# Kernel optimization log

Measured on AMD Instinct MI355X. Metric: run time of the kernel, lower is better.

## Reference

```python
import jax, jax.numpy as jnp
import numpy as np

N_HEADS = 16
D_MODEL = 1024
HEAD_DIM = D_MODEL // N_HEADS
B, S = 2, 2048


def setup_inputs() -> dict:
    key = jax.random.key(0)
    ks = jax.random.split(key, 10)
    scale = 1.0 / np.sqrt(D_MODEL)
    inp = {
        "query_tokens": jax.random.normal(ks[0], (B, S, D_MODEL), dtype=jnp.float32),
        "key_or_value_tokens": jax.random.normal(ks[1], (B, S, D_MODEL), dtype=jnp.float32),
        "mask": jnp.ones((B, S, S), dtype=jnp.int32),
        "Wq": jax.random.normal(ks[2], (D_MODEL, D_MODEL), dtype=jnp.float32) * scale,
        "bq": jnp.zeros((D_MODEL,), dtype=jnp.float32),
        "Wk": jax.random.normal(ks[3], (D_MODEL, D_MODEL), dtype=jnp.float32) * scale,
        "bk": jnp.zeros((D_MODEL,), dtype=jnp.float32),
        "Wv": jax.random.normal(ks[4], (D_MODEL, D_MODEL), dtype=jnp.float32) * scale,
        "bv": jnp.zeros((D_MODEL,), dtype=jnp.float32),
        "Wo": jax.random.normal(ks[5], (D_MODEL, D_MODEL), dtype=jnp.float32) * scale,
        "bo": jnp.zeros((D_MODEL,), dtype=jnp.float32),
    }
    return inp


def reference(query_tokens, key_or_value_tokens, mask, Wq, bq, Wk, bk, Wv, bv, Wo, bo):
    b, s, d = query_tokens.shape
    h, dh = N_HEADS, HEAD_DIM

    def proj(x, W, bias):
        # torch Linear: x @ W.T + b ; then split heads -> (b, h, s, dh)
        y = jnp.einsum("bsd,ed->bse", x, W) + bias
        return y.reshape(b, -1, h, dh).transpose(0, 2, 1, 3)

    q = proj(query_tokens, Wq, bq)
    k = proj(key_or_value_tokens, Wk, bk)
    v = proj(key_or_value_tokens, Wv, bv)

    scores = jnp.einsum("bhqd,bhkd->bhqk", q, k) / jnp.sqrt(jnp.float32(dh))
    # mask: (b, Sq, Sk) -> (b, 1, Sq, Sk); zeros get large negative fill
    scores = jnp.where(mask[:, None, :, :] == 0, jnp.float32(-1e9), scores)
    attn = jax.nn.softmax(scores, axis=-1)
    out = jnp.einsum("bhqk,bhkd->bhqd", attn, v)
    out = out.transpose(0, 2, 1, 3).reshape(b, s, d)
    return jnp.einsum("bsd,ed->bse", out, Wo) + bo
```

## Files before the change

### kernel.cpp

```cpp
#include <hip/hip_runtime.h>
#include <hip/hip_bf16.h>

typedef __bf16 bf16_8  __attribute__((ext_vector_type(8)));
typedef __bf16 bf16_4  __attribute__((ext_vector_type(4)));
typedef float  f32_4   __attribute__((ext_vector_type(4)));

#define NH 16
#define DHD 64
#define BB 2
#define SS 2048
#define DD 1024

__device__ __forceinline__ void gload16(const __bf16* g, __bf16* l) {
    __builtin_amdgcn_global_load_lds(
        (const __attribute__((address_space(1))) void*)g,
        (__attribute__((address_space(3))) void*)l, 16, 0, 0);
}

__global__ __launch_bounds__(256) void conv_all(
    const float* __restrict__ s0, const float* __restrict__ s1,
    const float* __restrict__ s2, const float* __restrict__ s3,
    const float* __restrict__ s4, const float* __restrict__ s5,
    __bf16* __restrict__ d0, __bf16* __restrict__ d1, __bf16* __restrict__ d2,
    __bf16* __restrict__ d3, __bf16* __restrict__ d4, __bf16* __restrict__ d5) {
    const int y = blockIdx.y;
    if (y >= 2 && blockIdx.x >= 1024) return;
    const float* s = (y == 0) ? s0 : (y == 1) ? s1 : (y == 2) ? s2
                   : (y == 3) ? s3 : (y == 4) ? s4 : s5;
    __bf16* d      = (y == 0) ? d0 : (y == 1) ? d1 : (y == 2) ? d2
                   : (y == 3) ? d3 : (y == 4) ? d4 : d5;
    const int i = (blockIdx.x * 256 + threadIdx.x) * 4;
    f32_4 v = *(const f32_4*)&s[i];
    bf16_4 o; o[0] = (__bf16)v[0]; o[1] = (__bf16)v[1];
    o[2] = (__bf16)v[2]; o[3] = (__bf16)v[3];
    *(bf16_4*)&d[i] = o;
}

__global__ __launch_bounds__(256) void mask_flags_k(const int* __restrict__ mask,
                                                    int* __restrict__ flags) {
    const int id = blockIdx.x;
    const int b = id >> 10, qt = (id >> 5) & 31, kt = id & 31;
    const int t = threadIdx.x;
    const int row = t >> 2, seg = t & 3;
    const int* p = mask + ((size_t)b * SS + qt * 64 + row) * SS + kt * 64 + seg * 16;
    int any0 = 0;
#pragma unroll
    for (int i = 0; i < 4; ++i) {
        int4 v = *(const int4*)&p[i * 4];
        any0 |= (v.x == 0) | (v.y == 0) | (v.z == 0) | (v.w == 0);
    }
    unsigned long long bal = __ballot(any0);
    __shared__ int sf[4];
    if ((t & 63) == 0) sf[t >> 6] = (bal != 0ULL);
    __syncthreads();
    if (t == 0) flags[id] = sf[0] | sf[1] | sf[2] | sf[3];
}

template <int LAYOUT>
__device__ __forceinline__ void gemm_body(const __bf16* __restrict__ A,
                                          const __bf16* __restrict__ W,
                                          const float* __restrict__ bias,
                                          __bf16* __restrict__ out,
                                          __bf16* ldsA, __bf16* ldsB) {
    const int tid  = threadIdx.x;
    const int lane = tid & 63;
    const int w    = tid >> 6;
    const int quad = lane >> 4;
    const int l15  = lane & 15;
    const int wm   = (w >> 1) * 64;
    const int wn   = (w & 1) * 64;
    const int m0   = blockIdx.x * 128;
    const int n0   = blockIdx.y * 128;

    f32_4 acc[4][4] = {};

    for (int kt = 0; kt < 1024; kt += 32) {
#pragma unroll
        for (int cc = 0; cc < 2; ++cc) {
            const int c   = tid + cc * 256;
            const int row = c >> 2;
            const int cp  = c & 3;
            gload16(&A[(size_t)(m0 + row) * 1024 + kt + cp * 8], &ldsA[c * 8]);
            gload16(&W[(size_t)(n0 + row) * 1024 + kt + cp * 8], &ldsB[c * 8]);
        }
        __syncthreads();

        bf16_8 af[4], bfr[4];
#pragma unroll
        for (int i = 0; i < 4; ++i)
            af[i] = *(const bf16_8*)&ldsA[(wm + i * 16 + l15) * 32 + quad * 8];
#pragma unroll
        for (int j = 0; j < 4; ++j)
            bfr[j] = *(const bf16_8*)&ldsB[(wn + j * 16 + l15) * 32 + quad * 8];
#pragma unroll
        for (int i = 0; i < 4; ++i)
#pragma unroll
            for (int j = 0; j < 4; ++j)
                acc[i][j] = __builtin_amdgcn_mfma_f32_16x16x32_bf16(
                    af[i], bfr[j], acc[i][j], 0, 0, 0);
        __syncthreads();
    }

#pragma unroll
    for (int i = 0; i < 4; ++i) {
#pragma unroll
        for (int j = 0; j < 4; ++j) {
            const int col = n0 + wn + j * 16 + l15;
            const float bv = bias[col];
            if (LAYOUT == 2) {
                const int row0 = m0 + wm + i * 16 + quad * 4;
                bf16_4 pk;
#pragma unroll
                for (int r = 0; r < 4; ++r) pk[r] = (__bf16)(acc[i][j][r] + bv);
                const int bb = row0 >> 11, s0 = row0 & 2047;
                const int h = col >> 6, dh = col & 63;
                *(bf16_4*)&out[(((size_t)bb * NH + h) * DHD + dh) * SS + s0] = pk;
            } else {
#pragma unroll
                for (int r = 0; r < 4; ++r) {
                    const int row = m0 + wm + i * 16 + quad * 4 + r;
                    out[(((size_t)(row >> 11) * NH + (col >> 6)) * SS +
                         (row & 2047)) * DHD + (col & 63)] =
                        (__bf16)(acc[i][j][r] + bv);
                }
            }
        }
    }
}

__global__ __launch_bounds__(256) void gemm_qkv(
    const __bf16* __restrict__ Xq, const __bf16* __restrict__ Xkv,
    const __bf16* __restrict__ Wq, const float* __restrict__ bq,
    const __bf16* __restrict__ Wk, const float* __restrict__ bk,
    const __bf16* __restrict__ Wv, const float* __restrict__ bv,
    __bf16* __restrict__ Qo, __bf16* __restrict__ Ko, __bf16* __restrict__ VTo) {
    __shared__ __align__(16) __bf16 ldsA[128 * 32];
    __shared__ __align__(16) __bf16 ldsB[128 * 32];
    const int z = blockIdx.z;
    const __bf16* A    = (z == 0) ? Xq : Xkv;
    const __bf16* W    = (z == 0) ? Wq : (z == 1 ? Wk : Wv);
    const float* bias  = (z == 0) ? bq : (z == 1 ? bk : bv);
    if (z == 2)
        gemm_body<2>(A, W, bias, VTo, ldsA, ldsB);
    else
        gemm_body<0>(A, W, bias, (z == 0) ? Qo : Ko, ldsA, ldsB);
}

__global__ __launch_bounds__(256) void gemm_final(
    const __bf16* __restrict__ A, const __bf16* __restrict__ W,
    const float* __restrict__ bias, float* __restrict__ out) {
    __shared__ __align__(16) __bf16 ldsA[64 * 32];
    __shared__ __align__(16) __bf16 ldsB[64 * 32];
    const int tid  = threadIdx.x;
    const int lane = tid & 63;
    const int w    = tid >> 6;
    const int quad = lane >> 4;
    const int l15  = lane & 15;
    const int wm   = (w >> 1) * 32;
    const int wn   = (w & 1) * 32;
    const int m0   = blockIdx.x * 64;
    const int n0   = blockIdx.y * 64;

    const int isB = w >> 1;
    const __bf16* src = isB ? W : A;
    const int     bN  = isB ? n0 : m0;
    __bf16*       dst = isB ? ldsB : ldsA;
    const int     w2  = w & 1;

    f32_4 acc[2][2] = {};

    for (int kt = 0; kt < 1024; kt += 32) {
#pragma unroll
        for (int cc = 0; cc < 2; ++cc) {
            const int c   = w2 * 128 + cc * 64 + lane;
            const int row = c >> 2;
            const int cp  = c & 3;
            gload16(&src[(size_t)(bN + row) * 1024 + kt + cp * 8], &dst[c * 8]);
        }
        __syncthreads();

        bf16_8 af[2], bfr[2];
#pragma unroll
        for (int i = 0; i < 2; ++i)
            af[i] = *(const bf16_8*)&ldsA[(wm + i * 16 + l15) * 32 + quad * 8];
#pragma unroll
        for (int j = 0; j < 2; ++j)
            bfr[j] = *(const bf16_8*)&ldsB[(wn + j * 16 + l15) * 32 + quad * 8];
#pragma unroll
        for (int i = 0; i < 2; ++i)
#pragma unroll
            for (int j = 0; j < 2; ++j)
                acc[i][j] = __builtin_amdgcn_mfma_f32_16x16x32_bf16(
                    af[i], bfr[j], acc[i][j], 0, 0, 0);
        __syncthreads();
    }

#pragma unroll
    for (int i = 0; i < 2; ++i)
#pragma unroll
        for (int j = 0; j < 2; ++j) {
            const int col = n0 + wn + j * 16 + l15;
            const float bv = bias[col];
#pragma unroll
            for (int r = 0; r < 4; ++r) {
                const int row = m0 + wm + i * 16 + quad * 4 + r;
                out[(size_t)row * 1024 + col] = acc[i][j][r] + bv;
            }
        }
}

__global__ __launch_bounds__(256, 2) void flash_attn(
    const __bf16* __restrict__ Q, const __bf16* __restrict__ K,
    const __bf16* __restrict__ VT, const int* __restrict__ mask,
    const int* __restrict__ flags, __bf16* __restrict__ O) {
    __shared__ __align__(16) __bf16 ldsK[64 * 72];
    __shared__ __align__(16) __bf16 ldsVT[64 * 72];
    __shared__ __align__(16) __bf16 ldsP[128 * 72];

    const int tid  = threadIdx.x;
    const int lane = tid & 63;
    const int w    = tid >> 6;
    const int quad = lane >> 4;
    const int l15  = lane & 15;
    const int q0   = blockIdx.x * 128;
    const int bh   = blockIdx.y;
    const int b    = bh >> 4;

    const __bf16* Qb  = Q + (size_t)bh * SS * DHD;
    const __bf16* Kb  = K + (size_t)bh * SS * DHD;
    const __bf16* VTb = VT + (size_t)bh * DHD * SS;
    const int*    mb  = mask + (size_t)b * SS * SS;
    const int*    flb = flags + (size_t)b * 1024 + blockIdx.x * 64;

    bf16_8 qa[2][2];
#pragma unroll
    for (int mt = 0; mt < 2; ++mt)
#pragma unroll
        for (int ks = 0; ks < 2; ++ks) {
            bf16_8 t = *(const bf16_8*)&Qb[(size_t)(q0 + w * 32 + mt * 16 + l15) * DHD +
                                           ks * 32 + quad * 8];
#pragma unroll
            for (int e = 0; e < 8; ++e)
                qa[mt][ks][e] = (__bf16)((float)t[e] * 0.18033688011112042f);
        }

    f32_4 of[2][4] = {};
    float li[2][4] = {};

    const int r0 = tid >> 3;
    const int r1 = r0 + 32;
    const int cp = tid & 7;
    uint4 kr0 = *(const uint4*)&Kb[(size_t)r0 * DHD + cp * 8];
    uint4 kr1 = *(const uint4*)&Kb[(size_t)r1 * DHD + cp * 8];
    uint4 vr0 = *(const uint4*)&VTb[(size_t)r0 * SS + cp * 8];
    uint4 vr1 = *(const uint4*)&VTb[(size_t)r1 * SS + cp * 8];

    for (int k0 = 0; k0 < SS; k0 += 64) {
        *(uint4*)&ldsK[r0 * 72 + cp * 8]  = kr0;
        *(uint4*)&ldsK[r1 * 72 + cp * 8]  = kr1;
        *(uint4*)&ldsVT[r0 * 72 + cp * 8] = vr0;
        *(uint4*)&ldsVT[r1 * 72 + cp * 8] = vr1;
        if (k0 + 64 < SS) {
            const int kn = k0 + 64;
            kr0 = *(const uint4*)&Kb[(size_t)(kn + r0) * DHD + cp * 8];
            kr1 = *(const uint4*)&Kb[(size_t)(kn + r1) * DHD + cp * 8];
            vr0 = *(const uint4*)&VTb[(size_t)r0 * SS + kn + cp * 8];
            vr1 = *(const uint4*)&VTb[(size_t)r1 * SS + kn + cp * 8];
        }
        __syncthreads();

        const bool msk = ((flb[k0 >> 6] | flb[32 + (k0 >> 6)]) != 0);

        f32_4 sa[2][4] = {};
#pragma unroll
        for (int ks = 0; ks < 2; ++ks) {
            bf16_8 kb[4];
#pragma unroll
            for (int j = 0; j < 4; ++j)
                kb[j] = *(const bf16_8*)&ldsK[(j * 16 + l15) * 72 + ks * 32 + quad * 8];
#pragma unroll
            for (int mt = 0; mt < 2; ++mt)
#pragma unroll
                for (int j = 0; j < 4; ++j)
                    sa[mt][j] = __builtin_amdgcn_mfma_f32_16x16x32_bf16(
                        qa[mt][ks], kb[j], sa[mt][j], 0, 0, 0);
        }

        if (msk) {
#pragma unroll
            for (int mt = 0; mt < 2; ++mt)
#pragma unroll
                for (int j = 0; j < 4; ++j)
#pragma unroll
                    for (int r = 0; r < 4; ++r) {
                        const int qg = q0 + w * 32 + mt * 16 + quad * 4 + r;
                        const int kg = k0 + j * 16 + l15;
                        if (mb[(size_t)qg * SS + kg] == 0) sa[mt][j][r] = -1e9f;
                    }
        }

#pragma unroll
        for (int mt = 0; mt < 2; ++mt)
#pragma unroll
            for (int j = 0; j < 4; ++j)
#pragma unroll
                for (int r = 0; r < 4; ++r) {
                    const float p = exp2f(sa[mt][j][r]);
                    li[mt][r] += p;
                    ldsP[(w * 32 + mt * 16 + quad * 4 + r) * 72 + j * 16 + l15] =
                        (__bf16)p;
                }
        __syncthreads();

#pragma unroll
        for (int ks2 = 0; ks2 < 2; ++ks2) {
            bf16_8 pa[2], vb[4];
#pragma unroll
            for (int mt = 0; mt < 2; ++mt)
                pa[mt] = *(const bf16_8*)&ldsP[(w * 32 + mt * 16 + l15) * 72 +
                                               ks2 * 32 + quad * 8];
#pragma unroll
            for (int jo = 0; jo < 4; ++jo)
                vb[jo] = *(const bf16_8*)&ldsVT[(jo * 16 + l15) * 72 +
                                                ks2 * 32 + quad * 8];
#pragma unroll
            for (int mt = 0; mt < 2; ++mt)
#pragma unroll
                for (int jo = 0; jo < 4; ++jo)
                    of[mt][jo] = __builtin_amdgcn_mfma_f32_16x16x32_bf16(
                        pa[mt], vb[jo], of[mt][jo], 0, 0, 0);
        }
        __syncthreads();
    }

    const int hcol = (bh & 15) * 64;
#pragma unroll
    for (int mt = 0; mt < 2; ++mt)
#pragma unroll
        for (int r = 0; r < 4; ++r) {
            float ls = li[mt][r];
            ls += __shfl_xor(ls, 1);
            ls += __shfl_xor(ls, 2);
            ls += __shfl_xor(ls, 4);
            ls += __shfl_xor(ls, 8);
            const float inv = 1.0f / fmaxf(ls, 1e-37f);
            const int qg = q0 + w * 32 + mt * 16 + quad * 4 + r;
#pragma unroll
            for (int jo = 0; jo < 4; ++jo)
                O[((size_t)b * SS + qg) * DD + hcol + jo * 16 + l15] =
                    (__bf16)(of[mt][jo][r] * inv);
        }
}


extern "C" void kernel_launch(void* const* d_in, const int* in_sizes, int n_in,
                              void* d_out, int out_size, void* d_ws, size_t ws_size,
                              hipStream_t stream) {
    const float* xq   = (const float*)d_in[0];
    const float* xkv  = (const float*)d_in[1];
    const int*   mask = (const int*)d_in[2];
    const float* Wq   = (const float*)d_in[3];
    const float* bq   = (const float*)d_in[4];
    const float* Wk   = (const float*)d_in[5];
    const float* bk   = (const float*)d_in[6];
    const float* Wv   = (const float*)d_in[7];
    const float* bv   = (const float*)d_in[8];
    const float* Wo   = (const float*)d_in[9];
    const float* bo   = (const float*)d_in[10];

    __bf16* ws = (__bf16*)d_ws;
    const size_t big = (size_t)BB * SS * DD;
    const size_t wsz = (size_t)DD * DD;
    __bf16* Qw   = ws;
    __bf16* Kw   = Qw + big;
    __bf16* VTw  = Kw + big;
    __bf16* Aw   = VTw + big;
    __bf16* Xqb  = Aw + big;
    __bf16* Xkvb = Xqb + big;
    __bf16* Wqb  = Xkvb + big;
    __bf16* Wkb  = Wqb + wsz;
    __bf16* Wvb  = Wkb + wsz;
    __bf16* Wob  = Wvb + wsz;
    int* flags   = (int*)(Wob + wsz);

    conv_all<<<dim3(4096, 6), dim3(256), 0, stream>>>(xq, xkv, Wq, Wk, Wv, Wo,
                                                      Xqb, Xkvb, Wqb, Wkb, Wvb, Wob);
    mask_flags_k<<<dim3(2048), dim3(256), 0, stream>>>(mask, flags);
    gemm_qkv<<<dim3(32, 8, 3), dim3(256), 0, stream>>>(Xqb, Xkvb, Wqb, bq, Wkb, bk,
                                                       Wvb, bv, Qw, Kw, VTw);
    flash_attn<<<dim3(SS / 128, BB * NH), dim3(256), 0, stream>>>(Qw, Kw, VTw, mask,
                                                                  flags, Aw);
    gemm_final<<<dim3(64, 16), dim3(256), 0, stream>>>(Aw, Wob, bo, (float*)d_out);
}
```

Before: 268.1 us.

## Fuse mask-flag scan into conversion kernel, enlarge output GEMM tile, pad P stride

```diff
diff --git a/kernel.cpp b/kernel.cpp
--- a/kernel.cpp
+++ b/kernel.cpp
@@ -17,13 +17,34 @@
         (__attribute__((address_space(3))) void*)l, 16, 0, 0);
 }
 
-__global__ __launch_bounds__(256) void conv_all(
+__global__ __launch_bounds__(256) void conv_flags(
     const float* __restrict__ s0, const float* __restrict__ s1,
     const float* __restrict__ s2, const float* __restrict__ s3,
     const float* __restrict__ s4, const float* __restrict__ s5,
     __bf16* __restrict__ d0, __bf16* __restrict__ d1, __bf16* __restrict__ d2,
-    __bf16* __restrict__ d3, __bf16* __restrict__ d4, __bf16* __restrict__ d5) {
+    __bf16* __restrict__ d3, __bf16* __restrict__ d4, __bf16* __restrict__ d5,
+    const int* __restrict__ mask, int* __restrict__ flags) {
     const int y = blockIdx.y;
+    if (y == 6) {
+        if (blockIdx.x >= 2048) return;
+        const int id = blockIdx.x;
+        const int b = id >> 10, qt = (id >> 5) & 31, kt = id & 31;
+        const int t = threadIdx.x;
+        const int row = t >> 2, seg = t & 3;
+        const int* p = mask + ((size_t)b * SS + qt * 64 + row) * SS + kt * 64 + seg * 16;
+        int any0 = 0;
+#pragma unroll
+        for (int i = 0; i < 4; ++i) {
+            int4 v = *(const int4*)&p[i * 4];
+            any0 |= (v.x == 0) | (v.y == 0) | (v.z == 0) | (v.w == 0);
+        }
+        unsigned long long bal = __ballot(any0);
+        __shared__ int sf[4];
+        if ((t & 63) == 0) sf[t >> 6] = (bal != 0ULL);
+        __syncthreads();
+        if (t == 0) flags[id] = sf[0] | sf[1] | sf[2] | sf[3];
+        return;
+    }
     if (y >= 2 && blockIdx.x >= 1024) return;
     const float* s = (y == 0) ? s0 : (y == 1) ? s1 : (y == 2) ? s2
                    : (y == 3) ? s3 : (y == 4) ? s4 : s5;
@@ -34,26 +55,6 @@
     bf16_4 o; o[0] = (__bf16)v[0]; o[1] = (__bf16)v[1];
     o[2] = (__bf16)v[2]; o[3] = (__bf16)v[3];
     *(bf16_4*)&d[i] = o;
-}
-
-__global__ __launch_bounds__(256) void mask_flags_k(const int* __restrict__ mask,
-                                                    int* __restrict__ flags) {
-    const int id = blockIdx.x;
-    const int b = id >> 10, qt = (id >> 5) & 31, kt = id & 31;
-    const int t = threadIdx.x;
-    const int row = t >> 2, seg = t & 3;
-    const int* p = mask + ((size_t)b * SS + qt * 64 + row) * SS + kt * 64 + seg * 16;
-    int any0 = 0;
-#pragma unroll
-    for (int i = 0; i < 4; ++i) {
-        int4 v = *(const int4*)&p[i * 4];
-        any0 |= (v.x == 0) | (v.y == 0) | (v.z == 0) | (v.w == 0);
-    }
-    unsigned long long bal = __ballot(any0);
-    __shared__ int sf[4];
-    if ((t & 63) == 0) sf[t >> 6] = (bal != 0ULL);
-    __syncthreads();
-    if (t == 0) flags[id] = sf[0] | sf[1] | sf[2] | sf[3];
 }
 
 template <int LAYOUT>
@@ -149,45 +150,41 @@
 __global__ __launch_bounds__(256) void gemm_final(
     const __bf16* __restrict__ A, const __bf16* __restrict__ W,
     const float* __restrict__ bias, float* __restrict__ out) {
-    __shared__ __align__(16) __bf16 ldsA[64 * 32];
+    __shared__ __align__(16) __bf16 ldsA[128 * 32];
     __shared__ __align__(16) __bf16 ldsB[64 * 32];
     const int tid  = threadIdx.x;
     const int lane = tid & 63;
     const int w    = tid >> 6;
     const int quad = lane >> 4;
     const int l15  = lane & 15;
-    const int wm   = (w >> 1) * 32;
+    const int wm   = (w >> 1) * 64;
     const int wn   = (w & 1) * 32;
-    const int m0   = blockIdx.x * 64;
+    const int m0   = blockIdx.x * 128;
     const int n0   = blockIdx.y * 64;
 
-    const int isB = w >> 1;
-    const __bf16* src = isB ? W : A;
-    const int     bN  = isB ? n0 : m0;
-    __bf16*       dst = isB ? ldsB : ldsA;
-    const int     w2  = w & 1;
-
-    f32_4 acc[2][2] = {};
+    f32_4 acc[4][2] = {};
 
     for (int kt = 0; kt < 1024; kt += 32) {
 #pragma unroll
         for (int cc = 0; cc < 2; ++cc) {
-            const int c   = w2 * 128 + cc * 64 + lane;
+            const int c   = tid + cc * 256;
             const int row = c >> 2;
             const int cp  = c & 3;
-            gload16(&src[(size_t)(bN + row) * 1024 + kt + cp * 8], &dst[c * 8]);
-        }
-        __syncthreads();
-
-        bf16_8 af[2], bfr[2];
-#pragma unroll
-        for (int i = 0; i < 2; ++i)
+            gload16(&A[(size_t)(m0 + row) * 1024 + kt + cp * 8], &ldsA[c * 8]);
+        }
+        gload16(&W[(size_t)(n0 + (tid >> 2)) * 1024 + kt + (tid & 3) * 8],
+                &ldsB[tid * 8]);
+        __syncthreads();
+
+        bf16_8 af[4], bfr[2];
+#pragma unroll
+        for (int i = 0; i < 4; ++i)
             af[i] = *(const bf16_8*)&ldsA[(wm + i * 16 + l15) * 32 + quad * 8];
 #pragma unroll
         for (int j = 0; j < 2; ++j)
             bfr[j] = *(const bf16_8*)&ldsB[(wn + j * 16 + l15) * 32 + quad * 8];
 #pragma unroll
-        for (int i = 0; i < 2; ++i)
+        for (int i = 0; i < 4; ++i)
 #pragma unroll
             for (int j = 0; j < 2; ++j)
                 acc[i][j] = __builtin_amdgcn_mfma_f32_16x16x32_bf16(
@@ -196,7 +193,7 @@
     }
 
 #pragma unroll
-    for (int i = 0; i < 2; ++i)
+    for (int i = 0; i < 4; ++i)
 #pragma unroll
         for (int j = 0; j < 2; ++j) {
             const int col = n0 + wn + j * 16 + l15;
@@ -209,13 +206,14 @@
         }
 }
 
+#define PST 76
 __global__ __launch_bounds__(256, 2) void flash_attn(
     const __bf16* __restrict__ Q, const __bf16* __restrict__ K,
     const __bf16* __restrict__ VT, const int* __restrict__ mask,
     const int* __restrict__ flags, __bf16* __restrict__ O) {
     __shared__ __align__(16) __bf16 ldsK[64 * 72];
     __shared__ __align__(16) __bf16 ldsVT[64 * 72];
-    __shared__ __align__(16) __bf16 ldsP[128 * 72];
+    __shared__ __align__(16) __bf16 ldsP[128 * PST];
 
     const int tid  = threadIdx.x;
     const int lane = tid & 63;
@@ -307,7 +305,7 @@
                 for (int r = 0; r < 4; ++r) {
                     const float p = exp2f(sa[mt][j][r]);
                     li[mt][r] += p;
-                    ldsP[(w * 32 + mt * 16 + quad * 4 + r) * 72 + j * 16 + l15] =
+                    ldsP[(w * 32 + mt * 16 + quad * 4 + r) * PST + j * 16 + l15] =
                         (__bf16)p;
                 }
         __syncthreads();
@@ -317,7 +315,7 @@
             bf16_8 pa[2], vb[4];
 #pragma unroll
             for (int mt = 0; mt < 2; ++mt)
-                pa[mt] = *(const bf16_8*)&ldsP[(w * 32 + mt * 16 + l15) * 72 +
+                pa[mt] = *(const bf16_8*)&ldsP[(w * 32 + mt * 16 + l15) * PST +
                                                ks2 * 32 + quad * 8];
 #pragma unroll
             for (int jo = 0; jo < 4; ++jo)
@@ -383,12 +381,11 @@
     __bf16* Wob  = Wvb + wsz;
     int* flags   = (int*)(Wob + wsz);
 
-    conv_all<<<dim3(4096, 6), dim3(256), 0, stream>>>(xq, xkv, Wq, Wk, Wv, Wo,
-                                                      Xqb, Xkvb, Wqb, Wkb, Wvb, Wob);
-    mask_flags_k<<<dim3(2048), dim3(256), 0, stream>>>(mask, flags);
+    conv_flags<<<dim3(4096, 7), dim3(256), 0, stream>>>(
+        xq, xkv, Wq, Wk, Wv, Wo, Xqb, Xkvb, Wqb, Wkb, Wvb, Wob, mask, flags);
     gemm_qkv<<<dim3(32, 8, 3), dim3(256), 0, stream>>>(Xqb, Xkvb, Wqb, bq, Wkb, bk,
                                                        Wvb, bv, Qw, Kw, VTw);
     flash_attn<<<dim3(SS / 128, BB * NH), dim3(256), 0, stream>>>(Qw, Kw, VTw, mask,
                                                                   flags, Aw);
-    gemm_final<<<dim3(64, 16), dim3(256), 0, stream>>>(Aw, Wob, bo, (float*)d_out);
-}
+    gemm_final<<<dim3(32, 16), dim3(256), 0, stream>>>(Aw, Wob, bo, (float*)d_out);
+}
```

Result: no change. 268.9 us (+0.3%).
